# Kernel optimization log

Hardware: AMD Instinct MI355X
Metric: run time of the kernel (lower is better)

Reference implementation:

```python
import jax, jax.numpy as jnp
import numpy as np

T = 16384
D_IN = 512
D_HID = 512
D_OUT = 512


def setup_inputs() -> dict:
    key = jax.random.key(0)
    ks = jax.random.split(key, 7)
    s_in = 1.0 / np.sqrt(D_IN)
    s_hid = 1.0 / np.sqrt(D_HID)
    xs = jax.random.normal(ks[0], (T, D_IN), dtype=jnp.float32)
    Wz = jax.random.uniform(ks[1], (D_HID, D_IN), jnp.float32, -s_in, s_in)
    bz = jax.random.uniform(ks[2], (D_HID,), jnp.float32, -s_in, s_in)
    Wh = jax.random.uniform(ks[3], (D_HID, D_IN), jnp.float32, -s_in, s_in)
    bh = jax.random.uniform(ks[4], (D_HID,), jnp.float32, -s_in, s_in)
    Wo = jax.random.uniform(ks[5], (D_OUT, D_HID), jnp.float32, -s_hid, s_hid)
    bo = jax.random.uniform(ks[6], (D_OUT,), jnp.float32, -s_hid, s_hid)
    return {"xs": xs, "Wz": Wz, "bz": bz, "Wh": Wh, "bh": bh, "Wo": Wo, "bo": bo}


def _combine(first, second):
    a0, b0 = first
    a1, b1 = second
    return (a0 * a1, a1 * b0 + b1)


def reference(xs, Wz, bz, Wh, bh, Wo, bo):
    # gates and candidate hidden states: [T, H]
    zs = jax.nn.sigmoid(xs @ Wz.T + bz)
    hs = xs @ Wh.T + bh
    # prepend identity element (a=1, b=0) for the h_0 = 0 initial state
    a = jnp.concatenate([jnp.ones((1, zs.shape[1]), zs.dtype), 1.0 - zs], axis=0)
    b = jnp.concatenate([jnp.zeros((1, zs.shape[1]), zs.dtype), zs * hs], axis=0)
    _, states = jax.lax.associative_scan(_combine, (a, b))  # [T+1, H]
    return states[1:] @ Wo.T + bo  # [T, D_OUT]
```

## Files before the change

### kernel.cpp

```cpp
#include <hip/hip_runtime.h>
#include <hip/hip_bf16.h>
#include <cstdint>
#include <cmath>

#define T_SEQ 16384
#define DMODEL 512
#define NCHUNK 512
#define LCHUNK 32
#define XS_N   (T_SEQ * DMODEL)
#define W_N    (DMODEL * DMODEL)
#define N4_XS  (XS_N / 4)
#define N4_W   (W_N / 4)
#define N4_TOT (N4_XS + 3 * N4_W)

typedef __bf16 bf16x8 __attribute__((ext_vector_type(8)));
typedef float  f32x4  __attribute__((ext_vector_type(4)));

using bf16 = __hip_bfloat16;

__device__ __forceinline__ void load_lds16(const void* g, void* l) {
    __builtin_amdgcn_global_load_lds((const __attribute__((address_space(1))) void*)g,
                                     (__attribute__((address_space(3))) void*)l,
                                     16, 0, 0);
}

__device__ __forceinline__ unsigned short f2bf(float f) {
    union { float f; unsigned u; } v; v.f = f;
    const unsigned r = (v.u + 0x7FFFu + ((v.u >> 16) & 1u)) >> 16;
    return (unsigned short)r;
}
__device__ __forceinline__ float bf2f(unsigned short u) {
    union { unsigned u; float f; } v; v.u = ((unsigned)u) << 16;
    return v.f;
}

__device__ __forceinline__ void comb(float& A, float& B, float fA, float fB,
                                     float sA, float sB) {
    A = fA * sA;
    B = sA * fB + sB;
}

__global__ __launch_bounds__(256) void k_convert(
    const float* __restrict__ xs, const float* __restrict__ Wz,
    const float* __restrict__ Wh, const float* __restrict__ Wo,
    bf16* __restrict__ xs_c, bf16* __restrict__ Wz_c,
    bf16* __restrict__ Wh_c, bf16* __restrict__ Wo_c)
{
    const int i = blockIdx.x * 256 + threadIdx.x;
    if (i >= N4_TOT) return;
    const float* src;
    bf16* dst;
    int o;
    if (i < N4_XS) { src = xs; dst = xs_c; o = i; }
    else {
        const int j = i - N4_XS;
        const int w = j >> 16;
        o = j & 65535;
        src = (w == 0) ? Wz : (w == 1) ? Wh : Wo;
        dst = (w == 0) ? Wz_c : (w == 1) ? Wh_c : Wo_c;
    }
    const float4 v = ((const float4*)src)[o];
    ushort4 r;
    r.x = f2bf(v.x); r.y = f2bf(v.y); r.z = f2bf(v.z); r.w = f2bf(v.w);
    ((ushort4*)dst)[o] = r;
}

__global__ __launch_bounds__(256, 2) void gemm_zh(
    const bf16* __restrict__ xs, const bf16* __restrict__ Wz, const float* __restrict__ bz,
    const bf16* __restrict__ Wh, const float* __restrict__ bh,
    unsigned int* __restrict__ ab_ws,
    float* __restrict__ Aagg, float* __restrict__ Bagg)
{
    __shared__ __bf16 As[128 * 64];
    __shared__ __bf16 Zs[128 * 64];
    __shared__ __bf16 Hs[128 * 64];

    const int tid  = threadIdx.x;
    const int bm   = blockIdx.x;
    const int bn   = blockIdx.y;
    const int lane = tid & 63;
    const int wave = tid >> 6;
    const int wm   = wave >> 1;
    const int wn   = wave & 1;

    f32x4 accz[4][4], acch[4][4];
    #pragma unroll
    for (int i = 0; i < 4; ++i)
        #pragma unroll
        for (int j = 0; j < 4; ++j) {
            accz[i][j] = (f32x4){0.f, 0.f, 0.f, 0.f};
            acch[i][j] = (f32x4){0.f, 0.f, 0.f, 0.f};
        }

    const int row0 = tid >> 3;
    const int k8   = tid & 7;

    const bf16* xg = xs + (size_t)(bm * 128) * DMODEL + k8 * 8;
    const bf16* zg = Wz + (size_t)(bn * 128) * DMODEL + k8 * 8;
    const bf16* hg = Wh + (size_t)(bn * 128) * DMODEL + k8 * 8;

    const int quad = lane >> 4;
    const int col  = lane & 15;

    for (int k0 = 0; k0 < DMODEL; k0 += 64) {
        #pragma unroll
        for (int it = 0; it < 4; ++it) {
            const int row   = row0 + it * 32;
            const int chunk = it * 256 + tid;
            load_lds16(xg + (size_t)row * DMODEL + k0, &As[chunk * 8]);
            load_lds16(zg + (size_t)row * DMODEL + k0, &Zs[chunk * 8]);
            load_lds16(hg + (size_t)row * DMODEL + k0, &Hs[chunk * 8]);
        }
        __syncthreads();

        #pragma unroll
        for (int kk = 0; kk < 2; ++kk) {
            const int kb = kk * 32 + quad * 8;
            bf16x8 af[4], zf[4], hf[4];
            #pragma unroll
            for (int i = 0; i < 4; ++i) {
                const int am  = wm * 64 + i * 16 + col;
                const int bnr = wn * 64 + i * 16 + col;
                af[i] = *(const bf16x8*)&As[am * 64 + kb];
                zf[i] = *(const bf16x8*)&Zs[bnr * 64 + kb];
                hf[i] = *(const bf16x8*)&Hs[bnr * 64 + kb];
            }
            #pragma unroll
            for (int i = 0; i < 4; ++i)
                #pragma unroll
                for (int j = 0; j < 4; ++j) {
                    accz[i][j] = __builtin_amdgcn_mfma_f32_16x16x32_bf16(af[i], zf[j], accz[i][j], 0, 0, 0);
                    acch[i][j] = __builtin_amdgcn_mfma_f32_16x16x32_bf16(af[i], hf[j], acch[i][j], 0, 0, 0);
                }
        }
        __syncthreads();
    }

    const int c_lo = bm * 4 + wm * 2;
    #pragma unroll
    for (int j = 0; j < 4; ++j) {
        const int n = bn * 128 + wn * 64 + j * 16 + col;
        const float bzv = bz[n];
        const float bhv = bh[n];
        float cA[4], cB[4];
        #pragma unroll
        for (int i = 0; i < 4; ++i) {
            const int mbase = bm * 128 + wm * 64 + i * 16 + quad * 4;
            float A = 1.f, B = 0.f;
            #pragma unroll
            for (int r = 0; r < 4; ++r) {
                const float zpre = accz[i][j][r] + bzv;
                const float hpre = acch[i][j][r] + bhv;
                const float z = 1.f / (1.f + __expf(-zpre));
                const float a = 1.f - z;
                const float b = z * hpre;
                const size_t idx = (size_t)(mbase + r) * DMODEL + n;
                ab_ws[idx] = (unsigned)f2bf(a) | ((unsigned)f2bf(b) << 16);
                A = a * A;
                B = a * B + b;
            }
            cA[i] = A; cB[i] = B;
        }
        #pragma unroll
        for (int i = 0; i < 4; ++i) {
            float pA = __shfl_xor(cA[i], 16);
            float pB = __shfl_xor(cB[i], 16);
            const bool hi1 = quad & 1;
            comb(cA[i], cB[i], hi1 ? pA : cA[i], hi1 ? pB : cB[i],
                               hi1 ? cA[i] : pA, hi1 ? cB[i] : pB);
            pA = __shfl_xor(cA[i], 32);
            pB = __shfl_xor(cB[i], 32);
            const bool hi2 = quad >> 1;
            comb(cA[i], cB[i], hi2 ? pA : cA[i], hi2 ? pB : cB[i],
                               hi2 ? cA[i] : pA, hi2 ? cB[i] : pB);
        }
        float Alo, Blo, Ahi, Bhi;
        comb(Alo, Blo, cA[0], cB[0], cA[1], cB[1]);
        comb(Ahi, Bhi, cA[2], cB[2], cA[3], cB[3]);
        if (quad == 0) {
            Aagg[(size_t)c_lo * DMODEL + n]       = Alo;
            Bagg[(size_t)c_lo * DMODEL + n]       = Blo;
            Aagg[(size_t)(c_lo + 1) * DMODEL + n] = Ahi;
            Bagg[(size_t)(c_lo + 1) * DMODEL + n] = Bhi;
        }
    }
}

__global__ __launch_bounds__(512) void scan_p2(
    const float* __restrict__ Aagg, const float* __restrict__ Bagg,
    float* __restrict__ Hpre)
{
    const int h = blockIdx.x;
    const int c = threadIdx.x;
    __shared__ float sA[NCHUNK], sB[NCHUNK];

    float A = Aagg[(size_t)c * DMODEL + h];
    float B = Bagg[(size_t)c * DMODEL + h];
    sA[c] = A; sB[c] = B;
    __syncthreads();

    for (int off = 1; off < NCHUNK; off <<= 1) {
        float pA = 1.f, pB = 0.f;
        if (c >= off) { pA = sA[c - off]; pB = sB[c - off]; }
        __syncthreads();
        const float nB = A * pB + B;
        const float nA = A * pA;
        A = nA; B = nB;
        sA[c] = A; sB[c] = B;
        __syncthreads();
    }
    const float hp = (c == 0) ? 0.f : sB[c - 1];
    Hpre[(size_t)c * DMODEL + h] = hp;
}

__global__ __launch_bounds__(256) void scan_p3(
    const unsigned int* __restrict__ ab_ws, const float* __restrict__ Hpre,
    unsigned short* __restrict__ states)
{
    const int tid = threadIdx.x;
    const int c   = blockIdx.x;
    const float2 hp = ((const float2*)(Hpre + (size_t)c * DMODEL))[tid];
    float H0 = hp.x, H1 = hp.y;
    const size_t rowbase = (size_t)(c * LCHUNK) * DMODEL;
    #pragma unroll 8
    for (int i = 0; i < LCHUNK; ++i) {
        const size_t row = rowbase + (size_t)i * DMODEL;
        const uint2 u = ((const uint2*)(ab_ws + row))[tid];
        const float a0 = bf2f((unsigned short)(u.x & 0xFFFFu));
        const float b0 = bf2f((unsigned short)(u.x >> 16));
        const float a1 = bf2f((unsigned short)(u.y & 0xFFFFu));
        const float b1 = bf2f((unsigned short)(u.y >> 16));
        H0 = a0 * H0 + b0;
        H1 = a1 * H1 + b1;
        ushort2 s; s.x = f2bf(H0); s.y = f2bf(H1);
        ((ushort2*)(states + row))[tid] = s;
    }
}

__global__ __launch_bounds__(256, 2) void gemm_out(
    const bf16* __restrict__ states, const bf16* __restrict__ Wo, const float* __restrict__ bo,
    float* __restrict__ out)
{
    __shared__ __bf16 As[128 * 64];
    __shared__ __bf16 Bs[128 * 64];

    const int tid  = threadIdx.x;
    const int bm   = blockIdx.x;
    const int bn   = blockIdx.y;
    const int lane = tid & 63;
    const int wave = tid >> 6;
    const int wm   = wave >> 1;
    const int wn   = wave & 1;

    f32x4 acc[4][4];
    #pragma unroll
    for (int i = 0; i < 4; ++i)
        #pragma unroll
        for (int j = 0; j < 4; ++j)
            acc[i][j] = (f32x4){0.f, 0.f, 0.f, 0.f};

    const int row0 = tid >> 3;
    const int k8   = tid & 7;

    const bf16* ag = states + (size_t)(bm * 128) * DMODEL + k8 * 8;
    const bf16* bg = Wo     + (size_t)(bn * 128) * DMODEL + k8 * 8;

    const int quad = lane >> 4;
    const int col  = lane & 15;

    for (int k0 = 0; k0 < DMODEL; k0 += 64) {
        #pragma unroll
        for (int it = 0; it < 4; ++it) {
            const int row   = row0 + it * 32;
            const int chunk = it * 256 + tid;
            load_lds16(ag + (size_t)row * DMODEL + k0, &As[chunk * 8]);
            load_lds16(bg + (size_t)row * DMODEL + k0, &Bs[chunk * 8]);
        }
        __syncthreads();

        #pragma unroll
        for (int kk = 0; kk < 2; ++kk) {
            const int kb = kk * 32 + quad * 8;
            bf16x8 af[4], bf[4];
            #pragma unroll
            for (int i = 0; i < 4; ++i) {
                af[i] = *(const bf16x8*)&As[(wm * 64 + i * 16 + col) * 64 + kb];
                bf[i] = *(const bf16x8*)&Bs[(wn * 64 + i * 16 + col) * 64 + kb];
            }
            #pragma unroll
            for (int i = 0; i < 4; ++i)
                #pragma unroll
                for (int j = 0; j < 4; ++j)
                    acc[i][j] = __builtin_amdgcn_mfma_f32_16x16x32_bf16(af[i], bf[j], acc[i][j], 0, 0, 0);
        }
        __syncthreads();
    }

    #pragma unroll
    for (int j = 0; j < 4; ++j) {
        const int n = bn * 128 + wn * 64 + j * 16 + col;
        const float bov = bo[n];
        #pragma unroll
        for (int i = 0; i < 4; ++i) {
            const int mbase = bm * 128 + wm * 64 + i * 16 + quad * 4;
            #pragma unroll
            for (int r = 0; r < 4; ++r)
                out[(size_t)(mbase + r) * DMODEL + n] = acc[i][j][r] + bov;
        }
    }
}

extern "C" void kernel_launch(void* const* d_in, const int* in_sizes, int n_in,
                              void* d_out, int out_size, void* d_ws, size_t ws_size,
                              hipStream_t stream)
{
    const float* xs = (const float*)d_in[0];
    const float* Wz = (const float*)d_in[1];
    const float* bz = (const float*)d_in[2];
    const float* Wh = (const float*)d_in[3];
    const float* bh = (const float*)d_in[4];
    const float* Wo = (const float*)d_in[5];
    const float* bo = (const float*)d_in[6];
    float* out = (float*)d_out;

    char* w = (char*)d_ws;
    bf16*  xs_c   = (bf16*) (w);
    bf16*  Wz_c   = (bf16*) (w + 16777216ull);
    bf16*  Wh_c   = (bf16*) (w + 17301504ull);
    bf16*  Wo_c   = (bf16*) (w + 17825792ull);
    unsigned int*   ab_ws  = (unsigned int*)  (w + 18350080ull);
    unsigned short* states = (unsigned short*)(w + 51904512ull);
    float* Aagg   = (float*)(w + 68681728ull);
    float* Bagg   = (float*)(w + 69730304ull);
    float* Hpre   = (float*)(w + 70778880ull);

    k_convert<<<(N4_TOT + 255) / 256, 256, 0, stream>>>(xs, Wz, Wh, Wo, xs_c, Wz_c, Wh_c, Wo_c);
    gemm_zh<<<dim3(128, 4), 256, 0, stream>>>(xs_c, Wz_c, bz, Wh_c, bh, ab_ws, Aagg, Bagg);
    scan_p2<<<DMODEL, NCHUNK, 0, stream>>>(Aagg, Bagg, Hpre);
    scan_p3<<<NCHUNK, 256, 0, stream>>>(ab_ws, Hpre, states);
    gemm_out<<<dim3(128, 4), 256, 0, stream>>>((const bf16*)states, Wo_c, bo, out);
}
```

Measured before the change: 152.3 us.

## Fuse xs fp32-to-bf16 conversion into gemm_zh and transpose chunk aggregates

```diff
diff --git a/kernel.cpp b/kernel.cpp
--- a/kernel.cpp
+++ b/kernel.cpp
@@ -7,11 +7,9 @@
 #define DMODEL 512
 #define NCHUNK 512
 #define LCHUNK 32
-#define XS_N   (T_SEQ * DMODEL)
 #define W_N    (DMODEL * DMODEL)
-#define N4_XS  (XS_N / 4)
 #define N4_W   (W_N / 4)
-#define N4_TOT (N4_XS + 3 * N4_W)
+#define N4_W3  (3 * N4_W)
 
 typedef __bf16 bf16x8 __attribute__((ext_vector_type(8)));
 typedef float  f32x4  __attribute__((ext_vector_type(4)));
@@ -40,25 +38,17 @@
     B = sA * fB + sB;
 }
 
-__global__ __launch_bounds__(256) void k_convert(
-    const float* __restrict__ xs, const float* __restrict__ Wz,
-    const float* __restrict__ Wh, const float* __restrict__ Wo,
-    bf16* __restrict__ xs_c, bf16* __restrict__ Wz_c,
-    bf16* __restrict__ Wh_c, bf16* __restrict__ Wo_c)
+__global__ __launch_bounds__(256) void k_convert_w(
+    const float* __restrict__ Wz, const float* __restrict__ Wh,
+    const float* __restrict__ Wo,
+    bf16* __restrict__ Wz_c, bf16* __restrict__ Wh_c, bf16* __restrict__ Wo_c)
 {
     const int i = blockIdx.x * 256 + threadIdx.x;
-    if (i >= N4_TOT) return;
-    const float* src;
-    bf16* dst;
-    int o;
-    if (i < N4_XS) { src = xs; dst = xs_c; o = i; }
-    else {
-        const int j = i - N4_XS;
-        const int w = j >> 16;
-        o = j & 65535;
-        src = (w == 0) ? Wz : (w == 1) ? Wh : Wo;
-        dst = (w == 0) ? Wz_c : (w == 1) ? Wh_c : Wo_c;
-    }
+    if (i >= N4_W3) return;
+    const int w = i >> 16;
+    const int o = i & 65535;
+    const float* src = (w == 0) ? Wz : (w == 1) ? Wh : Wo;
+    bf16* dst = (w == 0) ? Wz_c : (w == 1) ? Wh_c : Wo_c;
     const float4 v = ((const float4*)src)[o];
     ushort4 r;
     r.x = f2bf(v.x); r.y = f2bf(v.y); r.z = f2bf(v.z); r.w = f2bf(v.w);
@@ -66,10 +56,10 @@
 }
 
 __global__ __launch_bounds__(256, 2) void gemm_zh(
-    const bf16* __restrict__ xs, const bf16* __restrict__ Wz, const float* __restrict__ bz,
+    const float* __restrict__ xs, const bf16* __restrict__ Wz, const float* __restrict__ bz,
     const bf16* __restrict__ Wh, const float* __restrict__ bh,
     unsigned int* __restrict__ ab_ws,
-    float* __restrict__ Aagg, float* __restrict__ Bagg)
+    float* __restrict__ AaggT, float* __restrict__ BaggT)
 {
     __shared__ __bf16 As[128 * 64];
     __shared__ __bf16 Zs[128 * 64];
@@ -94,10 +84,12 @@
 
     const int row0 = tid >> 3;
     const int k8   = tid & 7;
-
-    const bf16* xg = xs + (size_t)(bm * 128) * DMODEL + k8 * 8;
     const bf16* zg = Wz + (size_t)(bn * 128) * DMODEL + k8 * 8;
     const bf16* hg = Wh + (size_t)(bn * 128) * DMODEL + k8 * 8;
+
+    const int frow = tid >> 4;
+    const int f4   = tid & 15;
+    const float* xg = xs + ((size_t)(bm * 128) + frow) * DMODEL + f4 * 4;
 
     const int quad = lane >> 4;
     const int col  = lane & 15;
@@ -107,9 +99,19 @@
         for (int it = 0; it < 4; ++it) {
             const int row   = row0 + it * 32;
             const int chunk = it * 256 + tid;
-            load_lds16(xg + (size_t)row * DMODEL + k0, &As[chunk * 8]);
             load_lds16(zg + (size_t)row * DMODEL + k0, &Zs[chunk * 8]);
             load_lds16(hg + (size_t)row * DMODEL + k0, &Hs[chunk * 8]);
+        }
+        #pragma unroll
+        for (int it2 = 0; it2 < 8; ++it2) {
+            const int row = frow + it2 * 16;
+            const float4 v = *(const float4*)(xg + (size_t)(it2 * 16) * DMODEL + k0);
+            __hip_bfloat162 p0 = __float22bfloat162_rn(make_float2(v.x, v.y));
+            __hip_bfloat162 p1 = __float22bfloat162_rn(make_float2(v.z, v.w));
+            uint2 pk;
+            pk.x = *(const unsigned*)&p0;
+            pk.y = *(const unsigned*)&p1;
+            *(uint2*)&As[row * 64 + f4 * 4] = pk;
         }
         __syncthreads();
 
@@ -178,24 +180,24 @@
         comb(Alo, Blo, cA[0], cB[0], cA[1], cB[1]);
         comb(Ahi, Bhi, cA[2], cB[2], cA[3], cB[3]);
         if (quad == 0) {
-            Aagg[(size_t)c_lo * DMODEL + n]       = Alo;
-            Bagg[(size_t)c_lo * DMODEL + n]       = Blo;
-            Aagg[(size_t)(c_lo + 1) * DMODEL + n] = Ahi;
-            Bagg[(size_t)(c_lo + 1) * DMODEL + n] = Bhi;
+            AaggT[(size_t)n * NCHUNK + c_lo]     = Alo;
+            BaggT[(size_t)n * NCHUNK + c_lo]     = Blo;
+            AaggT[(size_t)n * NCHUNK + c_lo + 1] = Ahi;
+            BaggT[(size_t)n * NCHUNK + c_lo + 1] = Bhi;
         }
     }
 }
 
 __global__ __launch_bounds__(512) void scan_p2(
-    const float* __restrict__ Aagg, const float* __restrict__ Bagg,
-    float* __restrict__ Hpre)
+    const float* __restrict__ AaggT, const float* __restrict__ BaggT,
+    float* __restrict__ HpreT)
 {
     const int h = blockIdx.x;
     const int c = threadIdx.x;
     __shared__ float sA[NCHUNK], sB[NCHUNK];
 
-    float A = Aagg[(size_t)c * DMODEL + h];
-    float B = Bagg[(size_t)c * DMODEL + h];
+    float A = AaggT[(size_t)h * NCHUNK + c];
+    float B = BaggT[(size_t)h * NCHUNK + c];
     sA[c] = A; sB[c] = B;
     __syncthreads();
 
@@ -210,17 +212,17 @@
         __syncthreads();
     }
     const float hp = (c == 0) ? 0.f : sB[c - 1];
-    Hpre[(size_t)c * DMODEL + h] = hp;
+    HpreT[(size_t)h * NCHUNK + c] = hp;
 }
 
 __global__ __launch_bounds__(256) void scan_p3(
-    const unsigned int* __restrict__ ab_ws, const float* __restrict__ Hpre,
+    const unsigned int* __restrict__ ab_ws, const float* __restrict__ HpreT,
     unsigned short* __restrict__ states)
 {
     const int tid = threadIdx.x;
     const int c   = blockIdx.x;
-    const float2 hp = ((const float2*)(Hpre + (size_t)c * DMODEL))[tid];
-    float H0 = hp.x, H1 = hp.y;
+    float H0 = HpreT[(size_t)(2 * tid) * NCHUNK + c];
+    float H1 = HpreT[(size_t)(2 * tid + 1) * NCHUNK + c];
     const size_t rowbase = (size_t)(c * LCHUNK) * DMODEL;
     #pragma unroll 8
     for (int i = 0; i < LCHUNK; ++i) {
@@ -324,19 +326,18 @@
     float* out = (float*)d_out;
 
     char* w = (char*)d_ws;
-    bf16*  xs_c   = (bf16*) (w);
-    bf16*  Wz_c   = (bf16*) (w + 16777216ull);
-    bf16*  Wh_c   = (bf16*) (w + 17301504ull);
-    bf16*  Wo_c   = (bf16*) (w + 17825792ull);
-    unsigned int*   ab_ws  = (unsigned int*)  (w + 18350080ull);
-    unsigned short* states = (unsigned short*)(w + 51904512ull);
-    float* Aagg   = (float*)(w + 68681728ull);
-    float* Bagg   = (float*)(w + 69730304ull);
-    float* Hpre   = (float*)(w + 70778880ull);
-
-    k_convert<<<(N4_TOT + 255) / 256, 256, 0, stream>>>(xs, Wz, Wh, Wo, xs_c, Wz_c, Wh_c, Wo_c);
-    gemm_zh<<<dim3(128, 4), 256, 0, stream>>>(xs_c, Wz_c, bz, Wh_c, bh, ab_ws, Aagg, Bagg);
-    scan_p2<<<DMODEL, NCHUNK, 0, stream>>>(Aagg, Bagg, Hpre);
-    scan_p3<<<NCHUNK, 256, 0, stream>>>(ab_ws, Hpre, states);
+    bf16*  Wz_c   = (bf16*) (w);
+    bf16*  Wh_c   = (bf16*) (w + 524288ull);
+    bf16*  Wo_c   = (bf16*) (w + 1048576ull);
+    unsigned int*   ab_ws  = (unsigned int*)  (w + 1572864ull);
+    unsigned short* states = (unsigned short*)(w + 35127296ull);
+    float* AaggT  = (float*)(w + 51904512ull);
+    float* BaggT  = (float*)(w + 52953088ull);
+    float* HpreT  = (float*)(w + 54001664ull);
+
+    k_convert_w<<<(N4_W3 + 255) / 256, 256, 0, stream>>>(Wz, Wh, Wo, Wz_c, Wh_c, Wo_c);
+    gemm_zh<<<dim3(128, 4), 256, 0, stream>>>(xs, Wz_c, bz, Wh_c, bh, ab_ws, AaggT, BaggT);
+    scan_p2<<<DMODEL, NCHUNK, 0, stream>>>(AaggT, BaggT, HpreT);
+    scan_p3<<<NCHUNK, 256, 0, stream>>>(ab_ws, HpreT, states);
     gemm_out<<<dim3(128, 4), 256, 0, stream>>>((const bf16*)states, Wo_c, bo, out);
 }
```

New measurement: 151.8 us. About the same (-0.3%).
